# Performance work log

Measured on AMD Instinct MI355X. Metric: run time of the kernel, lower is better.

## Reference

```python
import jax, jax.numpy as jnp
import numpy as np

NEG_FILL = -100.0  # matches torch new_full(-100.0) init for scatter-amax


def reference(x, part_labels, parts_num=16):
    # x: (n, c, s, h, w) float; part_labels: (n, s, h, w) int in [0, parts_num)
    n, c, s, h, w = x.shape
    hw = h * w
    ns = n * s
    # (n s) c (h w)
    feat = jnp.transpose(x, (0, 2, 1, 3, 4)).reshape(ns, c, hw)
    labels = part_labels.reshape(ns, hw).astype(jnp.int32)

    b3 = jnp.arange(ns)[:, None, None]          # (ns,1,1)
    ch = jnp.arange(c)[None, :, None]            # (1,c,1)
    lbl3 = labels[:, None, :]                    # (ns,1,hw) -> broadcasts to (ns,c,hw)

    pooled_sum = jnp.zeros((ns, c, parts_num), x.dtype).at[b3, ch, lbl3].add(feat)
    b2 = jnp.arange(ns)[:, None]
    pooled_count = jnp.zeros((ns, parts_num), x.dtype).at[b2, labels].add(1.0)  # (ns,P)
    pooled_max = jnp.full((ns, c, parts_num), NEG_FILL, x.dtype).at[b3, ch, lbl3].max(feat)

    count = pooled_count[:, None, :]             # (ns,1,P)
    pooled_mean = pooled_sum / jnp.maximum(count, 1.0)
    pooled_max = jnp.where(count > 0, pooled_max, 0.0)
    pooled = pooled_mean + pooled_max            # (ns,c,P)
    # (n s) c p -> n c s p
    return jnp.transpose(pooled.reshape(n, s, c, parts_num), (0, 2, 1, 3))


def setup_inputs() -> dict:
    key = jax.random.key(0)
    k1, k2 = jax.random.split(key)
    n, c, s, h, w = 16, 256, 32, 16, 11
    parts_num = 16
    x = jax.random.normal(k1, (n, c, s, h, w), dtype=jnp.float32)
    part_labels = jax.random.randint(k2, (n, s, h, w), 0, parts_num, dtype=jnp.int64)
    return {"x": x, "part_labels": part_labels, "parts_num": parts_num}
```

## Files before the change

### kernel.cpp

```cpp
#include <hip/hip_runtime.h>


constexpr int C   = 256;
constexpr int S   = 32;
constexpr int HW  = 176;
constexpr int P   = 16;
constexpr int ROW = S * HW;
constexpr int GC  = 16;
constexpr int PITCH = 178;
constexpr int BCAP  = 64;
constexpr float NEG_FILL = -100.0f;

__global__ __launch_bounds__(256) void hpp_kernel(
    const float* __restrict__ x,
    const int*   __restrict__ labels,
    float*       __restrict__ out)
{
    __shared__ float         tile[GC * PITCH];
    __shared__ unsigned char perm[P * BCAP];
    __shared__ int           cnt[P];

    const int tid = threadIdx.x;
    const int blk = blockIdx.x;
    const int ns  = blk >> 4, cg = blk & 15;
    const int n   = ns >> 5,  s  = ns & 31;

    const int* ln = labels + (size_t)ns * HW;
    int lab = 0;
    if (tid < HW) lab = ln[tid];

    const float* xb = x + (size_t)(n * C + cg * GC) * ROW + s * HW;
    const int f0 = tid, f1 = tid + 256, f2 = tid + 512;
    const int r0 = f0 / 44, j0 = f0 - r0 * 44;
    const int r1 = f1 / 44, j1 = f1 - r1 * 44;
    const int r2 = f2 / 44, j2 = f2 - r2 * 44;
    float4 v0 = *(const float4*)(xb + (size_t)r0 * ROW + j0 * 4);
    float4 v1 = *(const float4*)(xb + (size_t)r1 * ROW + j1 * 4);
    float4 v2 = make_float4(0.f, 0.f, 0.f, 0.f);
    const bool has2 = (f2 < GC * 44);
    if (has2) v2 = *(const float4*)(xb + (size_t)r2 * ROW + j2 * 4);

    ((unsigned*)perm)[tid] = 0u;
    if (tid < P) cnt[tid] = 0;
    __syncthreads();
    if (tid < HW) {
        int r = atomicAdd(&cnt[lab], 1);
        if (r < BCAP) perm[(lab << 6) + r] = (unsigned char)tid;
    }
    __syncthreads();

    {
        float2* t0 = (float2*)&tile[r0 * PITCH + j0 * 4];
        t0[0] = make_float2(v0.x, v0.y); t0[1] = make_float2(v0.z, v0.w);
        float2* t1 = (float2*)&tile[r1 * PITCH + j1 * 4];
        t1[0] = make_float2(v1.x, v1.y); t1[1] = make_float2(v1.z, v1.w);
        if (has2) {
            float2* t2 = (float2*)&tile[r2 * PITCH + j2 * 4];
            t2[0] = make_float2(v2.x, v2.y); t2[1] = make_float2(v2.z, v2.w);
        }
    }
    __syncthreads();

    const int p = tid >> 4, c = tid & 15;
    const int k = min(cnt[p], BCAP);
    const unsigned char* pp = &perm[p << 6];
    const float*         tc = &tile[c * PITCH];

    float s0 = 0.f, s1 = 0.f, m0 = NEG_FILL, m1 = NEG_FILL;
    const int kf = k & ~3;
    for (int j = 0; j < kf; j += 4) {
        unsigned u = *(const unsigned*)&pp[j];
        float a0 = tc[u & 0xFF];
        float a1 = tc[(u >> 8) & 0xFF];
        float a2 = tc[(u >> 16) & 0xFF];
        float a3 = tc[u >> 24];
        s0 += a0; m0 = fmaxf(m0, a0);
        s1 += a1; m1 = fmaxf(m1, a1);
        s0 += a2; m0 = fmaxf(m0, a2);
        s1 += a3; m1 = fmaxf(m1, a3);
    }
    if (kf < k) {
        unsigned u = *(const unsigned*)&pp[kf];
        float a0 = tc[u & 0xFF];
        float a1 = tc[(u >> 8) & 0xFF];
        float a2 = tc[(u >> 16) & 0xFF];
        s0 += a0; m0 = fmaxf(m0, a0);
        if (kf + 1 < k) { s1 += a1; m1 = fmaxf(m1, a1); }
        if (kf + 2 < k) { s0 += a2; m0 = fmaxf(m0, a2); }
    }

    float res = (k > 0) ? (s0 + s1) / (float)k + fmaxf(m0, m1) : 0.f;
    out[((size_t)(n * C + cg * GC + c) * S + s) * P + p] = res;
}

extern "C" void kernel_launch(void* const* d_in, const int* in_sizes, int n_in,
                              void* d_out, int out_size, void* d_ws, size_t ws_size,
                              hipStream_t stream) {
    const float* x      = (const float*)d_in[0];
    const int*   labels = (const int*)d_in[1];
    float*       out    = (float*)d_out;

    const int ns_total = in_sizes[1] / HW;
    const int nblk     = ns_total * (C / GC);
    hpp_kernel<<<nblk, 256, 0, stream>>>(x, labels, out);
}
```

Baseline: 135.6 us.

## Process four channel groups per block with register prefetch of next tile

Each block now handles four consecutive 16-channel groups instead of one, so labels are loaded and the per-part permutation is built once per four groups. The next group's global loads are issued into registers while the current tile is reduced, overlapping memory latency with the gather loop. Barriers become explicit lgkmcnt waits followed by s_barrier. The grid shrinks fourfold (2048 blocks), which lowers available parallelism and may hurt latency hiding on a memory-bound kernel.

```diff
diff --git a/kernel.cpp b/kernel.cpp
--- a/kernel.cpp
+++ b/kernel.cpp
@@ -7,9 +7,14 @@
 constexpr int P   = 16;
 constexpr int ROW = S * HW;
 constexpr int GC  = 16;
+constexpr int ITEMS = 4;
 constexpr int PITCH = 178;
 constexpr int BCAP  = 64;
 constexpr float NEG_FILL = -100.0f;
+
+__device__ __forceinline__ void barrier_lgkm() {
+    asm volatile("s_waitcnt lgkmcnt(0)\n\ts_barrier" ::: "memory");
+}
 
 __global__ __launch_bounds__(256) void hpp_kernel(
     const float* __restrict__ x,
@@ -22,75 +27,92 @@
 
     const int tid = threadIdx.x;
     const int blk = blockIdx.x;
-    const int ns  = blk >> 4, cg = blk & 15;
+    const int ns  = blk >> 2, qg = blk & 3;
     const int n   = ns >> 5,  s  = ns & 31;
 
     const int* ln = labels + (size_t)ns * HW;
     int lab = 0;
     if (tid < HW) lab = ln[tid];
 
-    const float* xb = x + (size_t)(n * C + cg * GC) * ROW + s * HW;
     const int f0 = tid, f1 = tid + 256, f2 = tid + 512;
     const int r0 = f0 / 44, j0 = f0 - r0 * 44;
     const int r1 = f1 / 44, j1 = f1 - r1 * 44;
     const int r2 = f2 / 44, j2 = f2 - r2 * 44;
-    float4 v0 = *(const float4*)(xb + (size_t)r0 * ROW + j0 * 4);
-    float4 v1 = *(const float4*)(xb + (size_t)r1 * ROW + j1 * 4);
+    const bool has2 = (f2 < GC * 44);
+
+    const float* xq = x + (size_t)(n * C + qg * (ITEMS * GC)) * ROW + s * HW;
+    const size_t o0 = (size_t)r0 * ROW + j0 * 4;
+    const size_t o1 = (size_t)r1 * ROW + j1 * 4;
+    const size_t o2 = (size_t)r2 * ROW + j2 * 4;
+
+    float4 v0 = *(const float4*)(xq + o0);
+    float4 v1 = *(const float4*)(xq + o1);
     float4 v2 = make_float4(0.f, 0.f, 0.f, 0.f);
-    const bool has2 = (f2 < GC * 44);
-    if (has2) v2 = *(const float4*)(xb + (size_t)r2 * ROW + j2 * 4);
+    if (has2) v2 = *(const float4*)(xq + o2);
 
     ((unsigned*)perm)[tid] = 0u;
     if (tid < P) cnt[tid] = 0;
-    __syncthreads();
+    barrier_lgkm();
     if (tid < HW) {
         int r = atomicAdd(&cnt[lab], 1);
         if (r < BCAP) perm[(lab << 6) + r] = (unsigned char)tid;
     }
-    __syncthreads();
-
-    {
-        float2* t0 = (float2*)&tile[r0 * PITCH + j0 * 4];
-        t0[0] = make_float2(v0.x, v0.y); t0[1] = make_float2(v0.z, v0.w);
-        float2* t1 = (float2*)&tile[r1 * PITCH + j1 * 4];
-        t1[0] = make_float2(v1.x, v1.y); t1[1] = make_float2(v1.z, v1.w);
-        if (has2) {
-            float2* t2 = (float2*)&tile[r2 * PITCH + j2 * 4];
-            t2[0] = make_float2(v2.x, v2.y); t2[1] = make_float2(v2.z, v2.w);
-        }
-    }
-    __syncthreads();
+    barrier_lgkm();
 
     const int p = tid >> 4, c = tid & 15;
     const int k = min(cnt[p], BCAP);
     const unsigned char* pp = &perm[p << 6];
     const float*         tc = &tile[c * PITCH];
+    float* op = out + ((size_t)(n * C + qg * (ITEMS * GC) + c) * S + s) * P + p;
 
-    float s0 = 0.f, s1 = 0.f, m0 = NEG_FILL, m1 = NEG_FILL;
-    const int kf = k & ~3;
-    for (int j = 0; j < kf; j += 4) {
-        unsigned u = *(const unsigned*)&pp[j];
-        float a0 = tc[u & 0xFF];
-        float a1 = tc[(u >> 8) & 0xFF];
-        float a2 = tc[(u >> 16) & 0xFF];
-        float a3 = tc[u >> 24];
-        s0 += a0; m0 = fmaxf(m0, a0);
-        s1 += a1; m1 = fmaxf(m1, a1);
-        s0 += a2; m0 = fmaxf(m0, a2);
-        s1 += a3; m1 = fmaxf(m1, a3);
+    #pragma unroll
+    for (int i = 0; i < ITEMS; ++i) {
+        {
+            float2* t0 = (float2*)&tile[r0 * PITCH + j0 * 4];
+            t0[0] = make_float2(v0.x, v0.y); t0[1] = make_float2(v0.z, v0.w);
+            float2* t1 = (float2*)&tile[r1 * PITCH + j1 * 4];
+            t1[0] = make_float2(v1.x, v1.y); t1[1] = make_float2(v1.z, v1.w);
+            if (has2) {
+                float2* t2 = (float2*)&tile[r2 * PITCH + j2 * 4];
+                t2[0] = make_float2(v2.x, v2.y); t2[1] = make_float2(v2.z, v2.w);
+            }
+        }
+        if (i + 1 < ITEMS) {
+            const float* xn = xq + (size_t)(i + 1) * GC * ROW;
+            v0 = *(const float4*)(xn + o0);
+            v1 = *(const float4*)(xn + o1);
+            if (has2) v2 = *(const float4*)(xn + o2);
+        }
+        barrier_lgkm();
+
+        float s0 = 0.f, s1 = 0.f, m0 = NEG_FILL, m1 = NEG_FILL;
+        const int kf = k & ~3;
+        for (int j = 0; j < kf; j += 4) {
+            unsigned u = *(const unsigned*)&pp[j];
+            float a0 = tc[u & 0xFF];
+            float a1 = tc[(u >> 8) & 0xFF];
+            float a2 = tc[(u >> 16) & 0xFF];
+            float a3 = tc[u >> 24];
+            s0 += a0; m0 = fmaxf(m0, a0);
+            s1 += a1; m1 = fmaxf(m1, a1);
+            s0 += a2; m0 = fmaxf(m0, a2);
+            s1 += a3; m1 = fmaxf(m1, a3);
+        }
+        if (kf < k) {
+            unsigned u = *(const unsigned*)&pp[kf];
+            float a0 = tc[u & 0xFF];
+            float a1 = tc[(u >> 8) & 0xFF];
+            float a2 = tc[(u >> 16) & 0xFF];
+            s0 += a0; m0 = fmaxf(m0, a0);
+            if (kf + 1 < k) { s1 += a1; m1 = fmaxf(m1, a1); }
+            if (kf + 2 < k) { s0 += a2; m0 = fmaxf(m0, a2); }
+        }
+
+        float res = (k > 0) ? (s0 + s1) / (float)k + fmaxf(m0, m1) : 0.f;
+        *op = res;
+        op += (size_t)GC * S * P;
+        if (i + 1 < ITEMS) barrier_lgkm();
     }
-    if (kf < k) {
-        unsigned u = *(const unsigned*)&pp[kf];
-        float a0 = tc[u & 0xFF];
-        float a1 = tc[(u >> 8) & 0xFF];
-        float a2 = tc[(u >> 16) & 0xFF];
-        s0 += a0; m0 = fmaxf(m0, a0);
-        if (kf + 1 < k) { s1 += a1; m1 = fmaxf(m1, a1); }
-        if (kf + 2 < k) { s0 += a2; m0 = fmaxf(m0, a2); }
-    }
-
-    float res = (k > 0) ? (s0 + s1) / (float)k + fmaxf(m0, m1) : 0.f;
-    out[((size_t)(n * C + cg * GC + c) * S + s) * P + p] = res;
 }
 
 extern "C" void kernel_launch(void* const* d_in, const int* in_sizes, int n_in,
@@ -101,6 +123,6 @@
     float*       out    = (float*)d_out;
 
     const int ns_total = in_sizes[1] / HW;
-    const int nblk     = ns_total * (C / GC);
+    const int nblk     = ns_total * ITEMS;
     hpp_kernel<<<nblk, 256, 0, stream>>>(x, labels, out);
 }
```

Result: slower. 140.6 us (+3.7%).
